# Kernel optimization log

Measured on AMD Instinct MI355X. Metric: run time of the kernel, lower is better.

The kernel has to match this reference:

```python
import jax, jax.numpy as jnp
import numpy as np


def extract_patches(x, k):
    # x: [B, C, H, W] -> patches [B, C, fh, fw, k, k]  (stride-1 VALID windows,
    # same layout as torch unfold(2,k,1).unfold(3,k,1))
    B, C, H, W = x.shape
    fh, fw = H - k + 1, W - k + 1
    rows = []
    for dy in range(k):  # k*k = 49 static slices, no data-dim python loop
        cols = [x[:, :, dy:dy + fh, dx:dx + fw] for dx in range(k)]
        rows.append(jnp.stack(cols, axis=-1))
    return jnp.stack(rows, axis=-2)  # [B, C, fh, fw, k, k]


def setup_inputs() -> dict:
    key = jax.random.key(0)
    k1, k2, k3 = jax.random.split(key, 3)
    B, Cin, H, W = 64, 3, 64, 64
    O, k = 16, 7
    stdv = 1.0 / float(np.sqrt(Cin * k * k))  # matches reset_parameters
    x = jax.random.normal(k1, (B, Cin, H, W), dtype=jnp.float32)
    K_hit = jax.random.uniform(k2, (O, Cin, k, k), jnp.float32, -stdv, stdv)
    K_miss = jax.random.uniform(k3, (O, Cin, k, k), jnp.float32, -stdv, stdv)
    return {"input": x, "K_hit": K_hit, "K_miss": K_miss}


def reference(input, K_hit, K_miss):
    B, Cin, H, W = input.shape
    O, _, k, _ = K_hit.shape
    fh = H - k + 1
    num_blocks = fh * fh * Cin  # as in the torch code (assumes square input)
    patches = extract_patches(input, k)  # [B, Cin, fh, fw, k, k]

    def body(carry, Ks):
        kh, km = Ks  # each [Cin, k, k]
        # F_hit = (patch - K_hit)*-1 ; (-relu(F_hit)).sum() == -sum(relu(K_hit - patch))
        s_hit = -jnp.sum(jax.nn.relu(kh[None, :, None, None, :, :] - patches))
        s_miss = jnp.sum(jax.nn.relu(patches - km[None, :, None, None, :, :]))
        return carry, (s_hit, s_miss)

    _, (s_hit, s_miss) = jax.lax.scan(body, None, (K_hit, K_miss))  # [O], [O]

    def tile(v):  # scalar per out channel broadcast over batch and all blocks
        t = jnp.broadcast_to(v[None, :, None], (B, O, num_blocks))
        return t.reshape(B, Cin * O, fh, fh)

    F_map = tile(s_hit - s_miss)
    F_hit_list = tile(s_hit)
    F_miss_list = tile(s_miss)
    return F_map, F_hit_list, F_miss_list
```

## Files before the change

kernel.cpp:

```cpp
#include <hip/hip_runtime.h>
#include <hip/hip_bf16.h>

#define NBUCK 2048
#define WB 0.005859375f
#define SCALE 170.6666667f

#define SEG 10092u
#define OSEG 161472u
#define OUT1 10334208u
#define NOUT 31002624u

#define TAIL_BASE (NOUT - 1310720u)
#define F_TR    0u
#define RC_TR   393408u
#define SF_OFF  983520u
#define SRC_OFF 983712u
#define PACK    984000u

typedef float v4f __attribute__((ext_vector_type(4)));

__device__ __forceinline__ void scan_store(
    float* sH, float* sWc, float* sWd, float* tail,
    unsigned baseT, int stride, int slot, unsigned baseS, int tid)
{
    const int lane = tid & 63;
    const int wid  = tid >> 6;
    const int b0 = 2 * tid, b1 = 2 * tid + 1;
    const float c0 = sH[b0], c1 = sH[b1];
    const float d0 = (float)b0 * c0, d1 = (float)b1 * c1;
    const float cs = c0 + c1, ds = d0 + d1;
    float ic = cs, id = ds;
#pragma unroll
    for (int off = 1; off < 64; off <<= 1) {
        const float tc = __shfl_up(ic, off);
        const float td = __shfl_up(id, off);
        if (lane >= off) { ic += tc; id += td; }
    }
    if (lane == 63) { sWc[wid] = ic; sWd[wid] = id; }
    __syncthreads();
    float baseC = 0.f, baseD = 0.f, Ntot = 0.f, Dtot = 0.f;
#pragma unroll
    for (int w = 0; w < 16; ++w) {
        const float wc = sWc[w], wd = sWd[w];
        Ntot += wc; Dtot += wd;
        if (w < wid) { baseC += wc; baseD += wd; }
    }
    const float Cex = baseC + ic - cs;
    const float Dex = baseD + id - ds;
    const float T0 = WB * (Dtot + 0.5f * Ntot);
    const float Tb0 = T0 + WB * (2.f * (float)b0 * Cex - 2.f * Dex - (float)b0 * Ntot);
    const float C1 = Cex + c0, D1 = Dex + d0;
    const float Tb1 = T0 + WB * (2.f * (float)b1 * C1 - 2.f * D1 - (float)b1 * Ntot);
    tail[baseT + (unsigned)b0 * stride + slot] = Tb0;
    tail[baseT + (unsigned)b1 * stride + slot] = Tb1;
    if (tid == 1023) {
        tail[baseT + (unsigned)NBUCK * stride + slot] =
            T0 + WB * ((float)NBUCK * Ntot - 2.f * Dtot);
        tail[baseS + slot] = T0 - 6.f * Ntot;
    }
}

__global__ __launch_bounds__(1024) void build_kernel(
    const float* __restrict__ x, float* __restrict__ tail, float* __restrict__ gsum)
{
    __shared__ float sH[NBUCK];
    __shared__ float sWc[16], sWd[16];
    const int blk = blockIdx.x;
    const int tid = threadIdx.x;
    sH[tid] = 0.f; sH[tid + 1024] = 0.f;
    if (blk == 0 && tid < 512) gsum[tid] = 0.f;
    __syncthreads();

    if (blk < 192) {
        const int batch = blk / 3, c = blk % 3;
        float4 val = ((const float4*)x)[blk * 1024 + tid];
        float vv[4] = {val.x, val.y, val.z, val.w};
        const int pix0 = tid * 4;
        const int py = pix0 >> 6;
#pragma unroll
        for (int e = 0; e < 4; ++e) {
            const int px = (pix0 & 63) + e;
            const float v = vv[e];
            const int b = min(max((int)fmaf(v, SCALE, 1024.f), 0), NBUCK - 1);
            atomicAdd(&sH[b], 1.f);
            const bool rb = (py < 6) | (py >= 58);
            const bool cb = (px < 6) | (px >= 58);
            if (rb & cb) {
                const int ri = (py < 6) ? py : py - 52;
                const int ci = (px < 6) ? px : px - 52;
                tail[PACK + ((unsigned)c * 144 + ri * 12 + ci) * 64u + batch] = v;
            }
        }
        __syncthreads();
        scan_store(sH, sWc, sWd, tail, F_TR, 192, c * 64 + batch, SF_OFF, tid);
    } else {
        const int u = blk - 192;
        const int c = u / 96;
        const int r2 = u - c * 96;
        const int kind = r2 / 48;
        const int r3 = r2 - kind * 48;
        const int i = r3 >> 2, qtr = r3 & 3;
        const int batch = qtr * 16 + (tid >> 6);
        const int pos = tid & 63;
        float v;
        if (kind == 0) {
            const int py = (i < 6) ? i : i + 52;
            v = x[(batch * 3 + c) * 4096 + py * 64 + pos];
        } else {
            const int px = (i < 6) ? i : i + 52;
            v = x[(batch * 3 + c) * 4096 + pos * 64 + px];
        }
        const int b = min(max((int)fmaf(v, SCALE, 1024.f), 0), NBUCK - 1);
        atomicAdd(&sH[b], 1.f);
        __syncthreads();
        scan_store(sH, sWc, sWd, tail, RC_TR, 288, u, SRC_OFF, tid);
    }
}

__global__ __launch_bounds__(512) void query_kernel(
    const float* __restrict__ Kh, const float* __restrict__ Km,
    const float* __restrict__ tail, float* __restrict__ gsum)
{
    __shared__ float sC[2304];
    __shared__ float sK[32];
    __shared__ float sredA[32][16];
    __shared__ float sredL[32][16];

    const int c  = blockIdx.x / 49;
    const int t  = blockIdx.x - c * 49;
    const int dy = t / 7, dx = t - dy * 7;
    const int tid = threadIdx.x;

    for (int i = tid; i < 576; i += 512) {
        const int cell = i >> 4, b4 = i & 15;
        const int qr = cell / 6, qc = cell - qr * 6;
        const int ri = (qr < dy) ? qr : 6 + qr;
        const int ci = (qc < dx) ? qc : 6 + qc;
        ((v4f*)sC)[i] = *(const v4f*)(tail + PACK +
            ((unsigned)c * 144 + ri * 12 + ci) * 64u + b4 * 4);
    }
    if (tid < 32)
        sK[tid] = ((tid >= 16) ? Km : Kh)[(tid & 15) * 147 + c * 49 + t];
    __syncthreads();

    const int q   = tid >> 4;
    const int sub = tid & 15;
    const float k = sK[q];

    float accA = 0.f, accL = 0.f;
#pragma unroll 16
    for (int step = 0; step < 144; ++step) {
        const float v = sC[sub + 16 * step];
        accA += fabsf(k - v);
        accL += k - v;
    }

    const float u = fmaf(k, SCALE, 1024.f);
    const int j = min(max((int)u, 0), NBUCK - 1);
    const float fr = u - (float)j;

    {
        const v4f f0 = *(const v4f*)(tail + F_TR + (unsigned)j * 192u + c * 64 + sub * 4);
        const v4f f1 = *(const v4f*)(tail + F_TR + (unsigned)(j + 1) * 192u + c * 64 + sub * 4);
        const float s0 = f0.x + f0.y + f0.z + f0.w;
        const float s1 = f1.x + f1.y + f1.z + f1.w;
        accA += s0 + fr * (s1 - s0);
        const v4f sf = *(const v4f*)(tail + SF_OFF + c * 64 + sub * 4);
        accL -= sf.x + sf.y + sf.z + sf.w;
        if (sub == 0) accL += k * 212992.f;
    }
    if (sub < 12) {
        int base_f4;
        if (sub < 6) {
            const int ri = (sub < dy) ? sub : 6 + sub;
            base_f4 = c * 96 + ri * 4;
        } else {
            const int s6 = sub - 6;
            const int ci = (s6 < dx) ? s6 : 6 + s6;
            base_f4 = c * 96 + 48 + ci * 4;
        }
        const v4f r0 = *(const v4f*)(tail + RC_TR + (unsigned)j * 288u + base_f4);
        const v4f r1 = *(const v4f*)(tail + RC_TR + (unsigned)(j + 1) * 288u + base_f4);
        const float s0 = r0.x + r0.y + r0.z + r0.w;
        const float s1 = r1.x + r1.y + r1.z + r1.w;
        accA -= s0 + fr * (s1 - s0);
        const v4f sr = *(const v4f*)(tail + SRC_OFF + base_f4);
        accL += sr.x + sr.y + sr.z + sr.w;
    }

    sredA[q][sub] = accA;
    sredL[q][sub] = accL;
    __syncthreads();
    if (tid < 64) {
        const int idx  = tid >> 1;
        const int part = tid & 1;
        const float (*sr)[16] = part ? sredL : sredA;
        float s = 0.f;
#pragma unroll
        for (int e = 0; e < 16; ++e) s += sr[idx][e];
        atomicAdd(&gsum[(blockIdx.x & 7) * 64 + part * 32 + idx], s);
    }
}

__global__ __launch_bounds__(256) void fill_kernel(
    const float* __restrict__ gsum, v4f* __restrict__ out, unsigned n4)
{
    __shared__ float sv[48];
    if (threadIdx.x < 48) {
        const int o = threadIdx.x & 15, grp = threadIdx.x >> 4;
        float Ah = 0.f, Am = 0.f, Lh = 0.f, Lm = 0.f;
#pragma unroll
        for (int b = 0; b < 8; ++b) {
            Ah += gsum[b * 64 + o];      Am += gsum[b * 64 + 16 + o];
            Lh += gsum[b * 64 + 32 + o]; Lm += gsum[b * 64 + 48 + o];
        }
        const float h = -0.5f * (Lh + Ah);
        const float m =  0.5f * (Am - Lm);
        sv[threadIdx.x] = (grp == 0) ? (h - m) : ((grp == 1) ? h : m);
    }
    __syncthreads();
    const unsigned stride = gridDim.x * blockDim.x;
    for (unsigned i = blockIdx.x * blockDim.x + threadIdx.x; i < n4; i += stride) {
        const unsigned f = i * 4u;
        const unsigned w   = f / OUT1;
        const unsigned rem = f - w * OUT1;
        const unsigned o   = (rem % OSEG) / SEG;
        const float val = sv[w * 16 + o];
        v4f pk = {val, val, val, val};
        __builtin_nontemporal_store(pk, &out[i]);
    }
}

extern "C" void kernel_launch(void* const* d_in, const int* in_sizes, int n_in,
                              void* d_out, int out_size, void* d_ws, size_t ws_size,
                              hipStream_t stream)
{
    const float* x  = (const float*)d_in[0];
    const float* Kh = (const float*)d_in[1];
    const float* Km = (const float*)d_in[2];
    float* out  = (float*)d_out;
    float* tail = out + TAIL_BASE;
    float* gsum = (float*)d_ws;

    build_kernel<<<480, 1024, 0, stream>>>(x, tail, gsum);
    query_kernel<<<147, 512, 0, stream>>>(Kh, Km, tail, gsum);
    fill_kernel <<<4096, 256, 0, stream>>>(gsum, (v4f*)out, NOUT / 4u);
}
```

Before: 50.83 us.

## Pre-reduce histogram tables across batch in a separate kernel before query

Histogram prefix tables are now stored one row per slot with a contiguous padded stride. A new reduce kernel sums them across batch (and groups the row/column strips) into compact per-channel tables. The query kernel then does single scalar lookups instead of strided vector gathers, and runs with 1024 threads so the direct patch loop is split in half per thread. The cost is an extra kernel launch, an extra pass over the tail buffer, and a serial dependency between kernels.

```diff
diff --git a/kernel.cpp b/kernel.cpp
--- a/kernel.cpp
+++ b/kernel.cpp
@@ -4,6 +4,7 @@
 #define NBUCK 2048
 #define WB 0.005859375f
 #define SCALE 170.6666667f
+#define ROWSTRIDE 2052u
 
 #define SEG 10092u
 #define OSEG 161472u
@@ -11,17 +12,17 @@
 #define NOUT 31002624u
 
 #define TAIL_BASE (NOUT - 1310720u)
-#define F_TR    0u
-#define RC_TR   393408u
-#define SF_OFF  983520u
-#define SRC_OFF 983712u
-#define PACK    984000u
+#define F_SLOT  0u
+#define RC_SLOT 393984u
+#define F_SUM   984960u
+#define RC_SUM  991116u
+#define PACK    1138860u
 
 typedef float v4f __attribute__((ext_vector_type(4)));
 
 __device__ __forceinline__ void scan_store(
     float* sH, float* sWc, float* sWd, float* tail,
-    unsigned baseT, int stride, int slot, unsigned baseS, int tid)
+    unsigned baseT, int slot, int tid)
 {
     const int lane = tid & 63;
     const int wid  = tid >> 6;
@@ -48,15 +49,13 @@
     const float Cex = baseC + ic - cs;
     const float Dex = baseD + id - ds;
     const float T0 = WB * (Dtot + 0.5f * Ntot);
-    const float Tb0 = T0 + WB * (2.f * (float)b0 * Cex - 2.f * Dex - (float)b0 * Ntot);
+    float* T = tail + baseT + (unsigned)slot * ROWSTRIDE;
+    T[b0] = T0 + WB * (2.f * (float)b0 * Cex - 2.f * Dex - (float)b0 * Ntot);
     const float C1 = Cex + c0, D1 = Dex + d0;
-    const float Tb1 = T0 + WB * (2.f * (float)b1 * C1 - 2.f * D1 - (float)b1 * Ntot);
-    tail[baseT + (unsigned)b0 * stride + slot] = Tb0;
-    tail[baseT + (unsigned)b1 * stride + slot] = Tb1;
+    T[b1] = T0 + WB * (2.f * (float)b1 * C1 - 2.f * D1 - (float)b1 * Ntot);
     if (tid == 1023) {
-        tail[baseT + (unsigned)NBUCK * stride + slot] =
-            T0 + WB * ((float)NBUCK * Ntot - 2.f * Dtot);
-        tail[baseS + slot] = T0 - 6.f * Ntot;
+        T[NBUCK] = T0 + WB * ((float)NBUCK * Ntot - 2.f * Dtot);
+        T[NBUCK + 1] = T0 - 6.f * Ntot;
     }
 }
 
@@ -92,7 +91,7 @@
             }
         }
         __syncthreads();
-        scan_store(sH, sWc, sWd, tail, F_TR, 192, c * 64 + batch, SF_OFF, tid);
+        scan_store(sH, sWc, sWd, tail, F_SLOT, c * 64 + batch, tid);
     } else {
         const int u = blk - 192;
         const int c = u / 96;
@@ -113,25 +112,56 @@
         const int b = min(max((int)fmaf(v, SCALE, 1024.f), 0), NBUCK - 1);
         atomicAdd(&sH[b], 1.f);
         __syncthreads();
-        scan_store(sH, sWc, sWd, tail, RC_TR, 288, u, SRC_OFF, tid);
-    }
-}
-
-__global__ __launch_bounds__(512) void query_kernel(
+        scan_store(sH, sWc, sWd, tail, RC_SLOT, u, tid);
+    }
+}
+
+__global__ __launch_bounds__(256) void reduce_kernel(float* __restrict__ tail)
+{
+    const int blk = blockIdx.x;
+    const int tid = threadIdx.x;
+    if (blk < 24) {
+        const int c = blk / 8, jc = blk % 8;
+        for (int jj = tid; jj < 257; jj += 256) {
+            const unsigned j = (unsigned)jc * 257u + jj;
+            if (j >= ROWSTRIDE) break;
+            float s = 0.f;
+#pragma unroll
+            for (int slot = 0; slot < 64; ++slot)
+                s += tail[F_SLOT + (unsigned)(c * 64 + slot) * ROWSTRIDE + j];
+            tail[F_SUM + (unsigned)c * ROWSTRIDE + j] = s;
+        }
+    } else {
+        const int r = blk - 24;
+        const int c = r / 24;
+        const int w24 = r - c * 24;
+        const int kind = w24 / 12, i = w24 - kind * 12;
+        const unsigned ubase = (unsigned)(c * 96 + kind * 48 + i * 4);
+        for (unsigned j = tid; j < ROWSTRIDE; j += 256) {
+            float s = 0.f;
+#pragma unroll
+            for (int q = 0; q < 4; ++q)
+                s += tail[RC_SLOT + (ubase + q) * ROWSTRIDE + j];
+            tail[RC_SUM + (unsigned)r * ROWSTRIDE + j] = s;
+        }
+    }
+}
+
+__global__ __launch_bounds__(1024) void query_kernel(
     const float* __restrict__ Kh, const float* __restrict__ Km,
     const float* __restrict__ tail, float* __restrict__ gsum)
 {
     __shared__ float sC[2304];
     __shared__ float sK[32];
-    __shared__ float sredA[32][16];
-    __shared__ float sredL[32][16];
+    __shared__ float sredA[32][32];
+    __shared__ float sredL[32][32];
 
     const int c  = blockIdx.x / 49;
     const int t  = blockIdx.x - c * 49;
     const int dy = t / 7, dx = t - dy * 7;
     const int tid = threadIdx.x;
 
-    for (int i = tid; i < 576; i += 512) {
+    for (int i = tid; i < 576; i += 1024) {
         const int cell = i >> 4, b4 = i & 15;
         const int qr = cell / 6, qc = cell - qr * 6;
         const int ri = (qr < dy) ? qr : 6 + qr;
@@ -143,14 +173,14 @@
         sK[tid] = ((tid >= 16) ? Km : Kh)[(tid & 15) * 147 + c * 49 + t];
     __syncthreads();
 
-    const int q   = tid >> 4;
-    const int sub = tid & 15;
+    const int q   = tid >> 5;
+    const int sub = tid & 31;
     const float k = sK[q];
 
     float accA = 0.f, accL = 0.f;
-#pragma unroll 16
-    for (int step = 0; step < 144; ++step) {
-        const float v = sC[sub + 16 * step];
+#pragma unroll 8
+    for (int step = 0; step < 72; ++step) {
+        const float v = sC[sub + 32 * step];
         accA += fabsf(k - v);
         accL += k - v;
     }
@@ -159,33 +189,24 @@
     const int j = min(max((int)u, 0), NBUCK - 1);
     const float fr = u - (float)j;
 
-    {
-        const v4f f0 = *(const v4f*)(tail + F_TR + (unsigned)j * 192u + c * 64 + sub * 4);
-        const v4f f1 = *(const v4f*)(tail + F_TR + (unsigned)(j + 1) * 192u + c * 64 + sub * 4);
-        const float s0 = f0.x + f0.y + f0.z + f0.w;
-        const float s1 = f1.x + f1.y + f1.z + f1.w;
-        accA += s0 + fr * (s1 - s0);
-        const v4f sf = *(const v4f*)(tail + SF_OFF + c * 64 + sub * 4);
-        accL -= sf.x + sf.y + sf.z + sf.w;
-        if (sub == 0) accL += k * 212992.f;
-    }
-    if (sub < 12) {
-        int base_f4;
-        if (sub < 6) {
-            const int ri = (sub < dy) ? sub : 6 + sub;
-            base_f4 = c * 96 + ri * 4;
+    if (sub == 0) {
+        const float* T = tail + F_SUM + (unsigned)c * ROWSTRIDE;
+        accA += T[j] + fr * (T[j + 1] - T[j]);
+        accL += k * 212992.f - T[NBUCK + 1];
+    } else if (sub <= 12) {
+        const int s12 = sub - 1;
+        int row;
+        if (s12 < 6) {
+            const int ri = (s12 < dy) ? s12 : 6 + s12;
+            row = c * 24 + ri;
         } else {
-            const int s6 = sub - 6;
+            const int s6 = s12 - 6;
             const int ci = (s6 < dx) ? s6 : 6 + s6;
-            base_f4 = c * 96 + 48 + ci * 4;
-        }
-        const v4f r0 = *(const v4f*)(tail + RC_TR + (unsigned)j * 288u + base_f4);
-        const v4f r1 = *(const v4f*)(tail + RC_TR + (unsigned)(j + 1) * 288u + base_f4);
-        const float s0 = r0.x + r0.y + r0.z + r0.w;
-        const float s1 = r1.x + r1.y + r1.z + r1.w;
-        accA -= s0 + fr * (s1 - s0);
-        const v4f sr = *(const v4f*)(tail + SRC_OFF + base_f4);
-        accL += sr.x + sr.y + sr.z + sr.w;
+            row = c * 24 + 12 + ci;
+        }
+        const float* T = tail + RC_SUM + (unsigned)row * ROWSTRIDE;
+        accA -= T[j] + fr * (T[j + 1] - T[j]);
+        accL += T[NBUCK + 1];
     }
 
     sredA[q][sub] = accA;
@@ -194,10 +215,10 @@
     if (tid < 64) {
         const int idx  = tid >> 1;
         const int part = tid & 1;
-        const float (*sr)[16] = part ? sredL : sredA;
+        const float (*sr)[32] = part ? sredL : sredA;
         float s = 0.f;
 #pragma unroll
-        for (int e = 0; e < 16; ++e) s += sr[idx][e];
+        for (int e = 0; e < 32; ++e) s += sr[idx][e];
         atomicAdd(&gsum[(blockIdx.x & 7) * 64 + part * 32 + idx], s);
     }
 }
@@ -242,7 +263,8 @@
     float* tail = out + TAIL_BASE;
     float* gsum = (float*)d_ws;
 
-    build_kernel<<<480, 1024, 0, stream>>>(x, tail, gsum);
-    query_kernel<<<147, 512, 0, stream>>>(Kh, Km, tail, gsum);
-    fill_kernel <<<4096, 256, 0, stream>>>(gsum, (v4f*)out, NOUT / 4u);
-}
+    build_kernel <<<480, 1024, 0, stream>>>(x, tail, gsum);
+    reduce_kernel<<<96, 256, 0, stream>>>(tail);
+    query_kernel <<<147, 1024, 0, stream>>>(Kh, Km, tail, gsum);
+    fill_kernel  <<<4096, 256, 0, stream>>>(gsum, (v4f*)out, NOUT / 4u);
+}
```

Measured after the change: 67.31 us. +32.4%, slower.
